# Optimization experiments

Hardware: AMD Instinct MI355X
Metric: run time of the kernel (lower is better)

## Reference

```python
import jax, jax.numpy as jnp
import numpy as np

N_NODES = 79
RAW_FEAT = 26
D_IN = RAW_FEAT + 6      # 32, in_channels after position concat
D_OUT = 2 * D_IN         # 64, out_channel_fac * in_channels
HIDDEN = 256
N_EDGES = 3000
BATCH = 256
POS_IDX = [120,124,128,132,136,140,144,148,152,237,241,245,249,253,257,261,265,269,354,358,362,366,370,374,378,382,386,471,475,479,483,487,491,495,499,503,588,592,596,600,604,608,612,616,620,705,709,713,717,721,725,729,733,737,822,826,830,834,838,842,846,850,854,48,53,60,67,73,157,352,388,583,586,817,901,906,913,920,926]


def _positions():
    width, height = 39, 25
    p = np.asarray(POS_IDX)
    xn = (p % width) / (width - 1)
    yn = (p // width) / (height - 1)
    feats = np.stack([xn, yn,
                      (np.sin(xn * 2 * np.pi) + 1) / 2,
                      (np.cos(xn * 2 * np.pi) + 1) / 2,
                      (np.sin(yn * 2 * np.pi) + 1) / 2,
                      (np.cos(yn * 2 * np.pi) + 1) / 2], axis=-1)
    return jnp.asarray(feats, jnp.float32)


def setup_inputs() -> dict:
    key = jax.random.key(0)
    ks = jax.random.split(key, 20)
    s = 0.05
    inp = {
        "state": jax.random.normal(ks[0], (BATCH, N_NODES, RAW_FEAT), jnp.float32),
        "pos_feat": _positions(),
        "edge_weights": jax.random.uniform(ks[1], (N_EDGES, 1), jnp.float32),
        # TransformerConv params (heads=1, edge_dim=1): torch Linear weights [out,in]
        "Wq": jax.random.normal(ks[2], (D_OUT, D_IN)) * s, "bq": jnp.zeros((D_OUT,)),
        "Wk": jax.random.normal(ks[3], (D_OUT, D_IN)) * s, "bk": jnp.zeros((D_OUT,)),
        "Wv": jax.random.normal(ks[4], (D_OUT, D_IN)) * s, "bv": jnp.zeros((D_OUT,)),
        "We": jax.random.normal(ks[5], (D_OUT, 1)) * s,            # lin_edge, bias=False
        "Wskip": jax.random.normal(ks[6], (D_OUT, D_IN)) * s, "bskip": jnp.zeros((D_OUT,)),
        # MLP head
        "W1": jax.random.normal(ks[7], (HIDDEN, D_IN + D_OUT + 1)) * s, "b1": jnp.zeros((HIDDEN,)),
        "g1": jnp.ones((HIDDEN,)), "beta1": jnp.zeros((HIDDEN,)),
        "W2": jax.random.normal(ks[8], (HIDDEN, HIDDEN)) * s, "b2": jnp.zeros((HIDDEN,)),
        "g2": jnp.ones((HIDDEN,)), "beta2": jnp.zeros((HIDDEN,)),
        "W3": jax.random.normal(ks[9], (1, HIDDEN)) * s, "b3": jnp.zeros((1,)),
        "edge_index": jax.random.randint(ks[10], (2, N_EDGES), 0, N_NODES, jnp.int32),
    }
    return inp


def _layernorm(x, g, b):
    m = x.mean(-1, keepdims=True)
    v = ((x - m) ** 2).mean(-1, keepdims=True)
    return (x - m) / jnp.sqrt(v + 1e-5) * g + b


def reference(state, pos_feat, edge_weights, Wq, bq, Wk, bk, Wv, bv, We, Wskip, bskip,
              W1, b1, g1, beta1, W2, b2, g2, beta2, W3, b3, edge_index):
    B = state.shape[0]
    # concat normalized positional features (shared across batch)
    x = jnp.concatenate([state, jnp.broadcast_to(pos_feat, (B, N_NODES, 6))], -1)  # [B,N,D_IN]
    src, dst = edge_index[0], edge_index[1]
    e = edge_weights @ We.T  # [E, D_OUT] edge embedding, shared across batch
    scale = 1.0 / jnp.sqrt(jnp.float32(D_OUT))

    def conv_one(xg):  # TransformerConv, heads=1, concat, root_weight
        q = xg @ Wq.T + bq
        k = xg @ Wk.T + bk
        v = xg @ Wv.T + bv
        ke = k[src] + e                      # [E, D_OUT]
        ve = v[src] + e
        alpha = (q[dst] * ke).sum(-1) * scale  # [E]
        amax = jax.ops.segment_max(alpha, dst, num_segments=N_NODES)
        amax = jnp.where(jnp.isfinite(amax), amax, 0.0)
        ex = jnp.exp(alpha - amax[dst])
        den = jax.ops.segment_sum(ex, dst, num_segments=N_NODES)
        w = ex / (den[dst] + 1e-16)
        agg = jax.ops.segment_sum(ve * w[:, None], dst, num_segments=N_NODES)
        return agg + xg @ Wskip.T + bskip

    out1 = jax.nn.relu(jax.vmap(conv_one)(x))  # [B,N,D_OUT]
    total_agents = x[..., 1].sum(-1)[:, None, None]  # [B,1,1]
    h = jnp.concatenate([out1, jnp.broadcast_to(total_agents, (B, N_NODES, 1)), x], -1)
    h = jax.nn.leaky_relu(_layernorm(h @ W1.T + b1, g1, beta1))
    h = jax.nn.leaky_relu(_layernorm(h @ W2.T + b2, g2, beta2))
    conc = jax.nn.softplus(h @ W3.T + b3).squeeze(-1)  # [B,N]
    action = conc / (conc.sum(-1, keepdims=True) + 1e-20)  # deterministic path
    return action
```

## Files before the change

kernel.cpp:

```cpp
#include <hip/hip_runtime.h>
#include <hip/hip_bf16.h>

#define N_NODES 79
#define RAW_FEAT 26
#define D_IN 32
#define D_OUT 64
#define HIDDEN 256
#define N_EDGES 3000
#define BATCH 256
#define M_ROWS (BATCH * N_NODES)
#define K1PAD 112

__global__ __launch_bounds__(256) void k_prep(
    const float* __restrict__ W1, const float* __restrict__ W2,
    const int* __restrict__ ei, const float* __restrict__ ew,
    const float* __restrict__ Wq, const float* __restrict__ Wk,
    const float* __restrict__ Wv, const float* __restrict__ Wsk,
    const float* __restrict__ bq, const float* __restrict__ bk,
    const float* __restrict__ bv, const float* __restrict__ bsk,
    float* __restrict__ W1t, float* __restrict__ W2t,
    float* __restrict__ Wall_t, float* __restrict__ ball,
    int* __restrict__ rp, int* __restrict__ csr_src,
    int* __restrict__ csr_dst, float* __restrict__ csr_ew)
{
    __shared__ float tile[64][65];
    __shared__ int cnt[N_NODES];
    __shared__ int base[N_NODES + 1];
    const int tid = threadIdx.x, bid = blockIdx.x;

    if (bid < 24) {
        const float* in; float* out; int C, Kpad, kb, rb;
        if (bid < 8) { in = W1; out = W1t; C = 97; Kpad = K1PAD;
                       kb = (bid & 1) * 64; rb = (bid >> 1) * 64; }
        else         { int b = bid - 8; in = W2; out = W2t; C = 256; Kpad = 256;
                       kb = (b & 3) * 64; rb = (b >> 2) * 64; }
        for (int i = tid; i < 4096; i += 256) {
            int rr = i >> 6, kk = i & 63;
            int r = rb + rr, k = kb + kk;
            tile[rr][kk] = (k < C) ? in[r * C + k] : 0.f;
        }
        __syncthreads();
        for (int i = tid; i < 4096; i += 256) {
            int kk = i >> 6, rr = i & 63;
            int k = kb + kk, r = rb + rr;
            if (k < Kpad) out[(size_t)k * HIDDEN + r] = tile[rr][kk];
        }
        return;
    }

    if (bid == 25) {
        for (int t = tid; t < 32 * 256; t += 256) {
            int k = t >> 8, j = t & 255;
            float v;
            if (j < 64)       v = Wq [j * 32 + k];
            else if (j < 128) v = Wk [(j - 64) * 32 + k];
            else if (j < 192) v = Wv [(j - 128) * 32 + k];
            else              v = Wsk[(j - 192) * 32 + k];
            Wall_t[t] = v;
        }
        if (tid < 64) {
            ball[tid]       = bq[tid];
            ball[64 + tid]  = bk[tid];
            ball[128 + tid] = bv[tid];
            ball[192 + tid] = bsk[tid];
        }
        return;
    }

    if (tid < N_NODES) cnt[tid] = 0;
    __syncthreads();
    for (int e = tid; e < N_EDGES; e += 256) atomicAdd(&cnt[ei[N_EDGES + e]], 1);
    __syncthreads();
    if (tid == 0) {
        int run = 0;
        for (int n = 0; n < N_NODES; ++n) { base[n] = run; run += cnt[n]; }
        base[N_NODES] = run;
    }
    __syncthreads();
    if (tid < N_NODES + 1) rp[tid] = base[tid];
    if (tid < N_NODES) cnt[tid] = base[tid];
    __syncthreads();
    for (int e = tid; e < N_EDGES; e += 256) {
        int d = ei[N_EDGES + e];
        int p = atomicAdd(&cnt[d], 1);
        csr_src[p] = ei[e];
        csr_dst[p] = d;
        csr_ew[p]  = ew[e];
    }
}

#define DOT4(S, Aa, Bb) S += Aa.x * Bb.x + Aa.y * Bb.y + Aa.z * Bb.z + Aa.w * Bb.w;

__global__ __launch_bounds__(256) void k_qkv(
    const float* __restrict__ state, const float* __restrict__ pos,
    const float* __restrict__ Wall_t, const float* __restrict__ ball,
    float* __restrict__ qkvs)
{
    __shared__ __align__(16) float Ax[32 * 32];
    __shared__ __align__(16) float Ws[32 * 256];

    const int tid = threadIdx.x;
    const int cg = tid & 31;
    const int rg = tid >> 5;
    const int m0 = blockIdx.x * 32;

    for (int t = tid; t < 32 * 32; t += 256) {
        int r = t >> 5, k = t & 31;
        int m = m0 + r, n = m - (m / N_NODES) * N_NODES;
        Ax[t] = (k < RAW_FEAT) ? state[m * RAW_FEAT + k] : pos[n * 6 + (k - RAW_FEAT)];
    }
    {
        const float4* Wg4 = (const float4*)Wall_t;
        float4* Ws4w = (float4*)Ws;
        #pragma unroll
        for (int i = 0; i < 8; ++i) Ws4w[tid + 256 * i] = Wg4[tid + 256 * i];
    }
    __syncthreads();

    float4 accL0 = {0,0,0,0}, accL1 = {0,0,0,0}, accL2 = {0,0,0,0}, accL3 = {0,0,0,0};
    float4 accH0 = {0,0,0,0}, accH1 = {0,0,0,0}, accH2 = {0,0,0,0}, accH3 = {0,0,0,0};
    const float4* Ax4 = (const float4*)Ax;
    const float4* Ws4 = (const float4*)Ws;

#define QSTEP(COMP, KS) { \
    float4 wL = Ws4[(kq * 4 + KS) * 64 + cg]; \
    float4 wH = Ws4[(kq * 4 + KS) * 64 + 32 + cg]; \
    accL0.x += a0.COMP * wL.x; accL0.y += a0.COMP * wL.y; accL0.z += a0.COMP * wL.z; accL0.w += a0.COMP * wL.w; \
    accL1.x += a1.COMP * wL.x; accL1.y += a1.COMP * wL.y; accL1.z += a1.COMP * wL.z; accL1.w += a1.COMP * wL.w; \
    accL2.x += a2.COMP * wL.x; accL2.y += a2.COMP * wL.y; accL2.z += a2.COMP * wL.z; accL2.w += a2.COMP * wL.w; \
    accL3.x += a3.COMP * wL.x; accL3.y += a3.COMP * wL.y; accL3.z += a3.COMP * wL.z; accL3.w += a3.COMP * wL.w; \
    accH0.x += a0.COMP * wH.x; accH0.y += a0.COMP * wH.y; accH0.z += a0.COMP * wH.z; accH0.w += a0.COMP * wH.w; \
    accH1.x += a1.COMP * wH.x; accH1.y += a1.COMP * wH.y; accH1.z += a1.COMP * wH.z; accH1.w += a1.COMP * wH.w; \
    accH2.x += a2.COMP * wH.x; accH2.y += a2.COMP * wH.y; accH2.z += a2.COMP * wH.z; accH2.w += a2.COMP * wH.w; \
    accH3.x += a3.COMP * wH.x; accH3.y += a3.COMP * wH.y; accH3.z += a3.COMP * wH.z; accH3.w += a3.COMP * wH.w; }

    #pragma unroll
    for (int kq = 0; kq < 8; ++kq) {
        float4 a0 = Ax4[(rg * 4 + 0) * 8 + kq];
        float4 a1 = Ax4[(rg * 4 + 1) * 8 + kq];
        float4 a2 = Ax4[(rg * 4 + 2) * 8 + kq];
        float4 a3 = Ax4[(rg * 4 + 3) * 8 + kq];
        QSTEP(x, 0)
        QSTEP(y, 1)
        QSTEP(z, 2)
        QSTEP(w, 3)
    }
#undef QSTEP

    {
        float4 bL = ((const float4*)ball)[cg];
        float4 bH = ((const float4*)ball)[32 + cg];
        float4* o4 = (float4*)qkvs;
#define QOUT(ACCL, ACCH, RR) { \
        float4 vL, vH; \
        vL.x = ACCL.x + bL.x; vL.y = ACCL.y + bL.y; vL.z = ACCL.z + bL.z; vL.w = ACCL.w + bL.w; \
        vH.x = ACCH.x + bH.x; vH.y = ACCH.y + bH.y; vH.z = ACCH.z + bH.z; vH.w = ACCH.w + bH.w; \
        o4[(size_t)(m0 + rg * 4 + RR) * 64 + cg] = vL; \
        o4[(size_t)(m0 + rg * 4 + RR) * 64 + 32 + cg] = vH; }
        QOUT(accL0, accH0, 0)
        QOUT(accL1, accH1, 1)
        QOUT(accL2, accH2, 2)
        QOUT(accL3, accH3, 3)
#undef QOUT
    }
}

__global__ __launch_bounds__(512) void k1_conv(
    const float* __restrict__ state, const float* __restrict__ qkvs,
    const int* __restrict__ rp_g, const int* __restrict__ csrc_g,
    const int* __restrict__ cdst_g, const float* __restrict__ cew_g,
    const float* __restrict__ We,
    float* __restrict__ out1_ws, float* __restrict__ ta_ws)
{
    __shared__ __align__(16) float qs [80 * 68];
    __shared__ __align__(16) float kss[80 * 68];
    __shared__ __align__(16) float vss[80 * 68];
    __shared__ __align__(16) float o1s[N_NODES * 68];
    __shared__ __align__(16) float SA[80 * 80];
    __shared__ __align__(16) float alpha[N_EDGES];
    __shared__ __align__(16) float ewc[N_EDGES];
    __shared__ unsigned short srcs[N_EDGES], dsts[N_EDGES];
    __shared__ __align__(16) float eW[64];
    __shared__ int   rp_s[80];
    __shared__ float qWe[80], csum_s[80];
    __shared__ float red80[80];

    const int b = blockIdx.x, tid = threadIdx.x;

    {
        const float4* qk4 = (const float4*)qkvs;
        for (int t = tid; t < N_NODES * 64; t += 512) {
            int n = t >> 6, j = t & 63;
            float4 v = qk4[(size_t)(b * N_NODES + n) * 64 + j];
            if (j < 16)      ((float4*)qs )[n * 17 + j]        = v;
            else if (j < 32) ((float4*)kss)[n * 17 + (j - 16)] = v;
            else if (j < 48) ((float4*)vss)[n * 17 + (j - 32)] = v;
            else             ((float4*)o1s)[n * 17 + (j - 48)] = v;
        }
    }
    for (int t = tid; t < N_EDGES; t += 512) {
        srcs[t] = (unsigned short)csrc_g[t];
        dsts[t] = (unsigned short)cdst_g[t];
        ewc[t]  = cew_g[t];
    }
    if (tid < 64) eW[tid] = We[tid];
    if (tid < 80) rp_s[tid] = rp_g[tid];
    if (tid < 79) red80[tid] = state[(b * N_NODES + tid) * RAW_FEAT + 1];
    if (tid == 79) red80[79] = 0.f;
    for (int t = tid; t < 68; t += 512) {
        qs[79 * 68 + t] = 0.f; kss[79 * 68 + t] = 0.f; vss[79 * 68 + t] = 0.f;
    }
    __syncthreads();

    for (int off = 64; off >= 1; off >>= 1) {
        if (tid < off && tid + off < 80) red80[tid] += red80[tid + off];
        __syncthreads();
    }
    if (tid == 0) ta_ws[b] = red80[0];

    if (tid < N_NODES) {
        const float4* q4 = (const float4*)(qs + tid * 68);
        const float4* e4 = (const float4*)eW;
        float s = 0.f;
        #pragma unroll
        for (int i = 0; i < 16; ++i) {
            float4 a = q4[i], e = e4[i];
            DOT4(s, a, e)
        }
        qWe[tid] = s;
    }
    __syncthreads();

    {
        const int rg = tid >> 5, cgp = tid & 31;
        const int r0 = rg * 5;
        int c0 = cgp * 3; if (c0 > 76) c0 = 76;
        float s00 = 0, s01 = 0, s02 = 0;
        float s10 = 0, s11 = 0, s12 = 0;
        float s20 = 0, s21 = 0, s22 = 0;
        float s30 = 0, s31 = 0, s32 = 0;
        float s40 = 0, s41 = 0, s42 = 0;
        const float4* q4p = (const float4*)qs;
        const float4* k4p = (const float4*)kss;
        for (int k4 = 0; k4 < 16; ++k4) {
            float4 q0 = q4p[(r0 + 0) * 17 + k4];
            float4 q1 = q4p[(r0 + 1) * 17 + k4];
            float4 q2 = q4p[(r0 + 2) * 17 + k4];
            float4 q3 = q4p[(r0 + 3) * 17 + k4];
            float4 q4v = q4p[(r0 + 4) * 17 + k4];
            float4 c0v = k4p[(c0 + 0) * 17 + k4];
            float4 c1v = k4p[(c0 + 1) * 17 + k4];
            float4 c2v = k4p[(c0 + 2) * 17 + k4];
            DOT4(s00, q0, c0v)  DOT4(s01, q0, c1v)  DOT4(s02, q0, c2v)
            DOT4(s10, q1, c0v)  DOT4(s11, q1, c1v)  DOT4(s12, q1, c2v)
            DOT4(s20, q2, c0v)  DOT4(s21, q2, c1v)  DOT4(s22, q2, c2v)
            DOT4(s30, q3, c0v)  DOT4(s31, q3, c1v)  DOT4(s32, q3, c2v)
            DOT4(s40, q4v, c0v) DOT4(s41, q4v, c1v) DOT4(s42, q4v, c2v)
        }
        SA[(r0 + 0) * 80 + c0 + 0] = s00; SA[(r0 + 0) * 80 + c0 + 1] = s01; SA[(r0 + 0) * 80 + c0 + 2] = s02;
        SA[(r0 + 1) * 80 + c0 + 0] = s10; SA[(r0 + 1) * 80 + c0 + 1] = s11; SA[(r0 + 1) * 80 + c0 + 2] = s12;
        SA[(r0 + 2) * 80 + c0 + 0] = s20; SA[(r0 + 2) * 80 + c0 + 1] = s21; SA[(r0 + 2) * 80 + c0 + 2] = s22;
        SA[(r0 + 3) * 80 + c0 + 0] = s30; SA[(r0 + 3) * 80 + c0 + 1] = s31; SA[(r0 + 3) * 80 + c0 + 2] = s32;
        SA[(r0 + 4) * 80 + c0 + 0] = s40; SA[(r0 + 4) * 80 + c0 + 1] = s41; SA[(r0 + 4) * 80 + c0 + 2] = s42;
    }
    __syncthreads();

    for (int t = tid; t < N_EDGES; t += 512) {
        int s = srcs[t], d = dsts[t];
        alpha[t] = 0.125f * (SA[d * 80 + s] + ewc[t] * qWe[d]);
    }
    __syncthreads();

    for (int t = tid; t < 6400; t += 512) SA[t] = 0.f;
    __syncthreads();

    if (tid < N_NODES) {
        int e0 = rp_s[tid], e1 = rp_s[tid + 1];
        float m = -1e30f;
        for (int e = e0; e < e1; ++e) m = fmaxf(m, alpha[e]);
        float s = 0.f, cs = 0.f;
        for (int e = e0; e < e1; ++e) {
            float ex = expf(alpha[e] - m);
            alpha[e] = ex;
            s += ex; cs += ex * ewc[e];
        }
        float rden = 1.f / (s + 1e-16f);
        csum_s[tid] = cs * rden;
        float* Ar = SA + tid * 80;
        for (int e = e0; e < e1; ++e) Ar[srcs[e]] += alpha[e] * rden;
    }
    __syncthreads();

    {
        const int rowg = tid >> 4, colg = tid & 15;
        int n0 = rowg * 3; if (n0 > 76) n0 = 76;
        float4 g0 = {0.f, 0.f, 0.f, 0.f};
        float4 g1 = {0.f, 0.f, 0.f, 0.f};
        float4 g2 = {0.f, 0.f, 0.f, 0.f};
        const float4* A4  = (const float4*)SA;
        const float4* v4p = (const float4*)vss;

#define AGGSTEP(COMP, SS) { \
        float4 vv = v4p[(s4 * 4 + SS) * 17 + colg]; \
        g0.x += a0.COMP * vv.x; g0.y += a0.COMP * vv.y; g0.z += a0.COMP * vv.z; g0.w += a0.COMP * vv.w; \
        g1.x += a1.COMP * vv.x; g1.y += a1.COMP * vv.y; g1.z += a1.COMP * vv.z; g1.w += a1.COMP * vv.w; \
        g2.x += a2.COMP * vv.x; g2.y += a2.COMP * vv.y; g2.z += a2.COMP * vv.z; g2.w += a2.COMP * vv.w; }

        for (int s4 = 0; s4 < 20; ++s4) {
            float4 a0 = A4[(n0 + 0) * 20 + s4];
            float4 a1 = A4[(n0 + 1) * 20 + s4];
            float4 a2 = A4[(n0 + 2) * 20 + s4];
            AGGSTEP(x, 0)
            AGGSTEP(y, 1)
            AGGSTEP(z, 2)
            AGGSTEP(w, 3)
        }
#undef AGGSTEP

        const float4* o4 = (const float4*)o1s;
        const float4* e4 = (const float4*)eW;
        float4 ev = e4[colg];

#define AGGOUT(GI, I) { int n = n0 + I; if (n < N_NODES) { \
        float4 sk = o4[n * 17 + colg]; float cs = csum_s[n]; float4 r; \
        r.x = fmaxf(sk.x + GI.x + cs * ev.x, 0.f); \
        r.y = fmaxf(sk.y + GI.y + cs * ev.y, 0.f); \
        r.z = fmaxf(sk.z + GI.z + cs * ev.z, 0.f); \
        r.w = fmaxf(sk.w + GI.w + cs * ev.w, 0.f); \
        ((float4*)out1_ws)[((size_t)b * N_NODES + n) * 16 + colg] = r; } }

        AGGOUT(g0, 0)
        AGGOUT(g1, 1)
        AGGOUT(g2, 2)
#undef AGGOUT
    }
}

__global__ __launch_bounds__(256) void k23_mlp(
    const float* __restrict__ state, const float* __restrict__ pos,
    const float* __restrict__ out1_ws, const float* __restrict__ ta_ws,
    const float* __restrict__ W1t, const float* __restrict__ b1,
    const float* __restrict__ g1, const float* __restrict__ be1,
    const float* __restrict__ W2t, const float* __restrict__ b2,
    const float* __restrict__ g2, const float* __restrict__ be2,
    const float* __restrict__ W3, const float* __restrict__ b3,
    float* __restrict__ conc_ws)
{
    __shared__ __align__(16) float A1[32 * K1PAD];
    __shared__ __align__(16) float A2[32 * 256];
    __shared__ __align__(16) float Ws[16 * 256];

    const int tid = threadIdx.x;
    const int cg = tid & 31;
    const int rg = tid >> 5;
    const int m0 = blockIdx.x * 32;

    const float4* W1t4 = (const float4*)W1t;
    const float4* W2t4 = (const float4*)W2t;
    const float4* A1_4 = (const float4*)A1;
    const float4* A2_4 = (const float4*)A2;
    float4* Ws4w = (float4*)Ws;
    const float4* Ws4 = (const float4*)Ws;

    for (int t = tid; t < 32 * K1PAD; t += 256) {
        int r = t / K1PAD, k = t - r * K1PAD;
        int m = m0 + r;
        float v = 0.f;
        if (k < 64)       v = out1_ws[m * 64 + k];
        else if (k == 64) v = ta_ws[m / N_NODES];
        else if (k < 91)  v = state[m * RAW_FEAT + (k - 65)];
        else if (k < 97)  { int n = m - (m / N_NODES) * N_NODES;
                            v = pos[n * 6 + (k - 91)]; }
        A1[t] = v;
    }
    float4 pre0 = W1t4[tid];
    float4 pre1 = W1t4[tid + 256];
    float4 pre2 = W1t4[tid + 512];
    float4 pre3 = W1t4[tid + 768];
    __syncthreads();

    float4 accL0 = {0,0,0,0}, accL1 = {0,0,0,0}, accL2 = {0,0,0,0}, accL3 = {0,0,0,0};
    float4 accH0 = {0,0,0,0}, accH1 = {0,0,0,0}, accH2 = {0,0,0,0}, accH3 = {0,0,0,0};

#define KSTEP(COMP, KS) { \
    float4 wL = Ws4[(kq * 4 + KS) * 64 + cg]; \
    float4 wH = Ws4[(kq * 4 + KS) * 64 + 32 + cg]; \
    accL0.x += a0.COMP * wL.x; accL0.y += a0.COMP * wL.y; accL0.z += a0.COMP * wL.z; accL0.w += a0.COMP * wL.w; \
    accL1.x += a1.COMP * wL.x; accL1.y += a1.COMP * wL.y; accL1.z += a1.COMP * wL.z; accL1.w += a1.COMP * wL.w; \
    accL2.x += a2.COMP * wL.x; accL2.y += a2.COMP * wL.y; accL2.z += a2.COMP * wL.z; accL2.w += a2.COMP * wL.w; \
    accL3.x += a3.COMP * wL.x; accL3.y += a3.COMP * wL.y; accL3.z += a3.COMP * wL.z; accL3.w += a3.COMP * wL.w; \
    accH0.x += a0.COMP * wH.x; accH0.y += a0.COMP * wH.y; accH0.z += a0.COMP * wH.z; accH0.w += a0.COMP * wH.w; \
    accH1.x += a1.COMP * wH.x; accH1.y += a1.COMP * wH.y; accH1.z += a1.COMP * wH.z; accH1.w += a1.COMP * wH.w; \
    accH2.x += a2.COMP * wH.x; accH2.y += a2.COMP * wH.y; accH2.z += a2.COMP * wH.z; accH2.w += a2.COMP * wH.w; \
    accH3.x += a3.COMP * wH.x; accH3.y += a3.COMP * wH.y; accH3.z += a3.COMP * wH.z; accH3.w += a3.COMP * wH.w; }

    for (int ch = 0; ch < 7; ++ch) {
        Ws4w[tid] = pre0; Ws4w[tid + 256] = pre1;
        Ws4w[tid + 512] = pre2; Ws4w[tid + 768] = pre3;
        __syncthreads();
        if (ch < 6) {
            pre0 = W1t4[(ch + 1) * 1024 + tid];
            pre1 = W1t4[(ch + 1) * 1024 + tid + 256];
            pre2 = W1t4[(ch + 1) * 1024 + tid + 512];
            pre3 = W1t4[(ch + 1) * 1024 + tid + 768];
        } else {
            pre0 = W2t4[tid];
            pre1 = W2t4[tid + 256];
            pre2 = W2t4[tid + 512];
            pre3 = W2t4[tid + 768];
        }
        #pragma unroll
        for (int kq = 0; kq < 4; ++kq) {
            float4 a0 = A1_4[(rg * 4 + 0) * 28 + ch * 4 + kq];
            float4 a1 = A1_4[(rg * 4 + 1) * 28 + ch * 4 + kq];
            float4 a2 = A1_4[(rg * 4 + 2) * 28 + ch * 4 + kq];
            float4 a3 = A1_4[(rg * 4 + 3) * 28 + ch * 4 + kq];
            KSTEP(x, 0)
            KSTEP(y, 1)
            KSTEP(z, 2)
            KSTEP(w, 3)
        }
        __syncthreads();
    }

    {
        float4 bL = ((const float4*)b1)[cg],  bH = ((const float4*)b1)[32 + cg];
        float4 gL = ((const float4*)g1)[cg],  gH = ((const float4*)g1)[32 + cg];
        float4 eL = ((const float4*)be1)[cg], eH = ((const float4*)be1)[32 + cg];

#define LN1_ROW(AL, AH, RR) { \
        float v0 = AL.x + bL.x, v1 = AL.y + bL.y, v2 = AL.z + bL.z, v3 = AL.w + bL.w; \
        float v4 = AH.x + bH.x, v5 = AH.y + bH.y, v6 = AH.z + bH.z, v7 = AH.w + bH.w; \
        float sm = v0 + v1 + v2 + v3 + v4 + v5 + v6 + v7; \
        float sq = v0*v0 + v1*v1 + v2*v2 + v3*v3 + v4*v4 + v5*v5 + v6*v6 + v7*v7; \
        for (int off = 16; off >= 1; off >>= 1) { sm += __shfl_xor(sm, off, 64); sq += __shfl_xor(sq, off, 64); } \
        float mu = sm * (1.f / 256.f), rstd = rsqrtf(sq * (1.f / 256.f) - mu * mu + 1e-5f); \
        float4 yL, yH; \
        yL.x = (v0 - mu) * rstd * gL.x + eL.x; yL.y = (v1 - mu) * rstd * gL.y + eL.y; \
        yL.z = (v2 - mu) * rstd * gL.z + eL.z; yL.w = (v3 - mu) * rstd * gL.w + eL.w; \
        yH.x = (v4 - mu) * rstd * gH.x + eH.x; yH.y = (v5 - mu) * rstd * gH.y + eH.y; \
        yH.z = (v6 - mu) * rstd * gH.z + eH.z; yH.w = (v7 - mu) * rstd * gH.w + eH.w; \
        yL.x = yL.x > 0.f ? yL.x : 0.01f * yL.x; yL.y = yL.y > 0.f ? yL.y : 0.01f * yL.y; \
        yL.z = yL.z > 0.f ? yL.z : 0.01f * yL.z; yL.w = yL.w > 0.f ? yL.w : 0.01f * yL.w; \
        yH.x = yH.x > 0.f ? yH.x : 0.01f * yH.x; yH.y = yH.y > 0.f ? yH.y : 0.01f * yH.y; \
        yH.z = yH.z > 0.f ? yH.z : 0.01f * yH.z; yH.w = yH.w > 0.f ? yH.w : 0.01f * yH.w; \
        ((float4*)A2)[(rg * 4 + RR) * 64 + cg] = yL; \
        ((float4*)A2)[(rg * 4 + RR) * 64 + 32 + cg] = yH; }

        LN1_ROW(accL0, accH0, 0)
        LN1_ROW(accL1, accH1, 1)
        LN1_ROW(accL2, accH2, 2)
        LN1_ROW(accL3, accH3, 3)
#undef LN1_ROW
        accL0 = {0,0,0,0}; accL1 = {0,0,0,0}; accL2 = {0,0,0,0}; accL3 = {0,0,0,0};
        accH0 = {0,0,0,0}; accH1 = {0,0,0,0}; accH2 = {0,0,0,0}; accH3 = {0,0,0,0};
    }

    for (int ch = 0; ch < 16; ++ch) {
        Ws4w[tid] = pre0; Ws4w[tid + 256] = pre1;
        Ws4w[tid + 512] = pre2; Ws4w[tid + 768] = pre3;
        __syncthreads();
        if (ch < 15) {
            pre0 = W2t4[(ch + 1) * 1024 + tid];
            pre1 = W2t4[(ch + 1) * 1024 + tid + 256];
            pre2 = W2t4[(ch + 1) * 1024 + tid + 512];
            pre3 = W2t4[(ch + 1) * 1024 + tid + 768];
        }
        #pragma unroll
        for (int kq = 0; kq < 4; ++kq) {
            float4 a0 = A2_4[(rg * 4 + 0) * 64 + ch * 4 + kq];
            float4 a1 = A2_4[(rg * 4 + 1) * 64 + ch * 4 + kq];
            float4 a2 = A2_4[(rg * 4 + 2) * 64 + ch * 4 + kq];
            float4 a3 = A2_4[(rg * 4 + 3) * 64 + ch * 4 + kq];
            KSTEP(x, 0)
            KSTEP(y, 1)
            KSTEP(z, 2)
            KSTEP(w, 3)
        }
        __syncthreads();
    }
#undef KSTEP

    {
        float4 bL = ((const float4*)b2)[cg],  bH = ((const float4*)b2)[32 + cg];
        float4 gL = ((const float4*)g2)[cg],  gH = ((const float4*)g2)[32 + cg];
        float4 eL = ((const float4*)be2)[cg], eH = ((const float4*)be2)[32 + cg];
        float4 wL3 = ((const float4*)W3)[cg], wH3 = ((const float4*)W3)[32 + cg];
        float bb3 = b3[0];

#define LN2_ROW(AL, AH, RR) { \
        float v0 = AL.x + bL.x, v1 = AL.y + bL.y, v2 = AL.z + bL.z, v3 = AL.w + bL.w; \
        float v4 = AH.x + bH.x, v5 = AH.y + bH.y, v6 = AH.z + bH.z, v7 = AH.w + bH.w; \
        float sm = v0 + v1 + v2 + v3 + v4 + v5 + v6 + v7; \
        float sq = v0*v0 + v1*v1 + v2*v2 + v3*v3 + v4*v4 + v5*v5 + v6*v6 + v7*v7; \
        for (int off = 16; off >= 1; off >>= 1) { sm += __shfl_xor(sm, off, 64); sq += __shfl_xor(sq, off, 64); } \
        float mu = sm * (1.f / 256.f), rstd = rsqrtf(sq * (1.f / 256.f) - mu * mu + 1e-5f); \
        float z0 = (v0 - mu) * rstd * gL.x + eL.x, z1 = (v1 - mu) * rstd * gL.y + eL.y; \
        float z2 = (v2 - mu) * rstd * gL.z + eL.z, z3 = (v3 - mu) * rstd * gL.w + eL.w; \
        float z4 = (v4 - mu) * rstd * gH.x + eH.x, z5 = (v5 - mu) * rstd * gH.y + eH.y; \
        float z6 = (v6 - mu) * rstd * gH.z + eH.z, z7 = (v7 - mu) * rstd * gH.w + eH.w; \
        z0 = z0 > 0.f ? z0 : 0.01f * z0; z1 = z1 > 0.f ? z1 : 0.01f * z1; \
        z2 = z2 > 0.f ? z2 : 0.01f * z2; z3 = z3 > 0.f ? z3 : 0.01f * z3; \
        z4 = z4 > 0.f ? z4 : 0.01f * z4; z5 = z5 > 0.f ? z5 : 0.01f * z5; \
        z6 = z6 > 0.f ? z6 : 0.01f * z6; z7 = z7 > 0.f ? z7 : 0.01f * z7; \
        float part = z0 * wL3.x + z1 * wL3.y + z2 * wL3.z + z3 * wL3.w \
                   + z4 * wH3.x + z5 * wH3.y + z6 * wH3.z + z7 * wH3.w; \
        for (int off = 16; off >= 1; off >>= 1) part += __shfl_xor(part, off, 64); \
        if (cg == 0) { float x = part + bb3; \
            conc_ws[m0 + rg * 4 + RR] = fmaxf(x, 0.f) + log1pf(expf(-fabsf(x))); } }

        LN2_ROW(accL0, accH0, 0)
        LN2_ROW(accL1, accH1, 1)
        LN2_ROW(accL2, accH2, 2)
        LN2_ROW(accL3, accH3, 3)
#undef LN2_ROW
    }
}

__global__ __launch_bounds__(128) void k4_norm(
    const float* __restrict__ conc_ws, float* __restrict__ out)
{
    __shared__ float red[128];
    const int b = blockIdx.x, tid = threadIdx.x;
    float v = 0.f;
    if (tid < N_NODES) v = conc_ws[b * N_NODES + tid];
    red[tid] = v;
    __syncthreads();
    for (int off = 64; off >= 1; off >>= 1) {
        if (tid < off) red[tid] += red[tid + off];
        __syncthreads();
    }
    float s = red[0];
    if (tid < N_NODES) out[b * N_NODES + tid] = v / (s + 1e-20f);
}

extern "C" void kernel_launch(void* const* d_in, const int* in_sizes, int n_in,
                              void* d_out, int out_size, void* d_ws, size_t ws_size,
                              hipStream_t stream) {
    const float* state = (const float*)d_in[0];
    const float* pos   = (const float*)d_in[1];
    const float* ew    = (const float*)d_in[2];
    const float* Wq  = (const float*)d_in[3];  const float* bq  = (const float*)d_in[4];
    const float* Wk  = (const float*)d_in[5];  const float* bk  = (const float*)d_in[6];
    const float* Wv  = (const float*)d_in[7];  const float* bv  = (const float*)d_in[8];
    const float* We  = (const float*)d_in[9];
    const float* Wsk = (const float*)d_in[10]; const float* bsk = (const float*)d_in[11];
    const float* W1  = (const float*)d_in[12]; const float* b1  = (const float*)d_in[13];
    const float* g1  = (const float*)d_in[14]; const float* be1 = (const float*)d_in[15];
    const float* W2  = (const float*)d_in[16]; const float* b2  = (const float*)d_in[17];
    const float* g2  = (const float*)d_in[18]; const float* be2 = (const float*)d_in[19];
    const float* W3  = (const float*)d_in[20]; const float* b3  = (const float*)d_in[21];
    const int*   ei  = (const int*)d_in[22];

    float* ws    = (float*)d_ws;
    float* ta    = ws;
    float* out1  = ws + 256;
    float* conc  = out1 + (size_t)M_ROWS * 64;
    float* W1t   = conc + M_ROWS;
    float* W2t   = W1t + K1PAD * HIDDEN;
    float* Wall  = W2t + HIDDEN * HIDDEN;
    float* ball  = Wall + 32 * 256;
    float* qkvs  = ball + 256;
    int*   rp    = (int*)(qkvs + (size_t)M_ROWS * 256);
    int*   csrc  = rp + 80;
    int*   cdst  = csrc + N_EDGES;
    float* cew   = (float*)(cdst + N_EDGES);
    float* out   = (float*)d_out;

    k_prep<<<dim3(26), dim3(256), 0, stream>>>(
        W1, W2, ei, ew, Wq, Wk, Wv, Wsk, bq, bk, bv, bsk,
        W1t, W2t, Wall, ball, rp, csrc, cdst, cew);
    k_qkv<<<dim3(M_ROWS / 32), dim3(256), 0, stream>>>(
        state, pos, Wall, ball, qkvs);
    k1_conv<<<dim3(BATCH), dim3(512), 0, stream>>>(
        state, qkvs, rp, csrc, cdst, cew, We, out1, ta);
    k23_mlp<<<dim3(M_ROWS / 32), dim3(256), 0, stream>>>(
        state, pos, out1, ta, W1t, b1, g1, be1,
        W2t, b2, g2, be2, W3, b3, conc);
    k4_norm<<<dim3(BATCH), dim3(128), 0, stream>>>(conc, out);
}
```

Measured before the change: 235.5 us.

## Fuse QKV projection into graph conv kernel and alias shared buffers

Removes the separate k_qkv kernel and computes the Q/K/V/skip projections inside k1_conv per batch block. Each block loads the block's node features and the weights into a shared union buffer that is later reused for SA and alpha. This drops one kernel launch and the write and re-read of a roughly 20 MB qkvs intermediate. It also merges A1/A2 in k23_mlp into one buffer to cut shared memory use. In exchange the projection runs on only 256 blocks with a simple per-thread GEMV loop, so it gets less parallelism than the standalone kernel had.

```diff
diff --git a/kernel.cpp b/kernel.cpp
--- a/kernel.cpp
+++ b/kernel.cpp
@@ -91,82 +91,9 @@
 
 #define DOT4(S, Aa, Bb) S += Aa.x * Bb.x + Aa.y * Bb.y + Aa.z * Bb.z + Aa.w * Bb.w;
 
-__global__ __launch_bounds__(256) void k_qkv(
+__global__ __launch_bounds__(512) void k1_conv(
     const float* __restrict__ state, const float* __restrict__ pos,
     const float* __restrict__ Wall_t, const float* __restrict__ ball,
-    float* __restrict__ qkvs)
-{
-    __shared__ __align__(16) float Ax[32 * 32];
-    __shared__ __align__(16) float Ws[32 * 256];
-
-    const int tid = threadIdx.x;
-    const int cg = tid & 31;
-    const int rg = tid >> 5;
-    const int m0 = blockIdx.x * 32;
-
-    for (int t = tid; t < 32 * 32; t += 256) {
-        int r = t >> 5, k = t & 31;
-        int m = m0 + r, n = m - (m / N_NODES) * N_NODES;
-        Ax[t] = (k < RAW_FEAT) ? state[m * RAW_FEAT + k] : pos[n * 6 + (k - RAW_FEAT)];
-    }
-    {
-        const float4* Wg4 = (const float4*)Wall_t;
-        float4* Ws4w = (float4*)Ws;
-        #pragma unroll
-        for (int i = 0; i < 8; ++i) Ws4w[tid + 256 * i] = Wg4[tid + 256 * i];
-    }
-    __syncthreads();
-
-    float4 accL0 = {0,0,0,0}, accL1 = {0,0,0,0}, accL2 = {0,0,0,0}, accL3 = {0,0,0,0};
-    float4 accH0 = {0,0,0,0}, accH1 = {0,0,0,0}, accH2 = {0,0,0,0}, accH3 = {0,0,0,0};
-    const float4* Ax4 = (const float4*)Ax;
-    const float4* Ws4 = (const float4*)Ws;
-
-#define QSTEP(COMP, KS) { \
-    float4 wL = Ws4[(kq * 4 + KS) * 64 + cg]; \
-    float4 wH = Ws4[(kq * 4 + KS) * 64 + 32 + cg]; \
-    accL0.x += a0.COMP * wL.x; accL0.y += a0.COMP * wL.y; accL0.z += a0.COMP * wL.z; accL0.w += a0.COMP * wL.w; \
-    accL1.x += a1.COMP * wL.x; accL1.y += a1.COMP * wL.y; accL1.z += a1.COMP * wL.z; accL1.w += a1.COMP * wL.w; \
-    accL2.x += a2.COMP * wL.x; accL2.y += a2.COMP * wL.y; accL2.z += a2.COMP * wL.z; accL2.w += a2.COMP * wL.w; \
-    accL3.x += a3.COMP * wL.x; accL3.y += a3.COMP * wL.y; accL3.z += a3.COMP * wL.z; accL3.w += a3.COMP * wL.w; \
-    accH0.x += a0.COMP * wH.x; accH0.y += a0.COMP * wH.y; accH0.z += a0.COMP * wH.z; accH0.w += a0.COMP * wH.w; \
-    accH1.x += a1.COMP * wH.x; accH1.y += a1.COMP * wH.y; accH1.z += a1.COMP * wH.z; accH1.w += a1.COMP * wH.w; \
-    accH2.x += a2.COMP * wH.x; accH2.y += a2.COMP * wH.y; accH2.z += a2.COMP * wH.z; accH2.w += a2.COMP * wH.w; \
-    accH3.x += a3.COMP * wH.x; accH3.y += a3.COMP * wH.y; accH3.z += a3.COMP * wH.z; accH3.w += a3.COMP * wH.w; }
-
-    #pragma unroll
-    for (int kq = 0; kq < 8; ++kq) {
-        float4 a0 = Ax4[(rg * 4 + 0) * 8 + kq];
-        float4 a1 = Ax4[(rg * 4 + 1) * 8 + kq];
-        float4 a2 = Ax4[(rg * 4 + 2) * 8 + kq];
-        float4 a3 = Ax4[(rg * 4 + 3) * 8 + kq];
-        QSTEP(x, 0)
-        QSTEP(y, 1)
-        QSTEP(z, 2)
-        QSTEP(w, 3)
-    }
-#undef QSTEP
-
-    {
-        float4 bL = ((const float4*)ball)[cg];
-        float4 bH = ((const float4*)ball)[32 + cg];
-        float4* o4 = (float4*)qkvs;
-#define QOUT(ACCL, ACCH, RR) { \
-        float4 vL, vH; \
-        vL.x = ACCL.x + bL.x; vL.y = ACCL.y + bL.y; vL.z = ACCL.z + bL.z; vL.w = ACCL.w + bL.w; \
-        vH.x = ACCH.x + bH.x; vH.y = ACCH.y + bH.y; vH.z = ACCH.z + bH.z; vH.w = ACCH.w + bH.w; \
-        o4[(size_t)(m0 + rg * 4 + RR) * 64 + cg] = vL; \
-        o4[(size_t)(m0 + rg * 4 + RR) * 64 + 32 + cg] = vH; }
-        QOUT(accL0, accH0, 0)
-        QOUT(accL1, accH1, 1)
-        QOUT(accL2, accH2, 2)
-        QOUT(accL3, accH3, 3)
-#undef QOUT
-    }
-}
-
-__global__ __launch_bounds__(512) void k1_conv(
-    const float* __restrict__ state, const float* __restrict__ qkvs,
     const int* __restrict__ rp_g, const int* __restrict__ csrc_g,
     const int* __restrict__ cdst_g, const float* __restrict__ cew_g,
     const float* __restrict__ We,
@@ -176,8 +103,7 @@
     __shared__ __align__(16) float kss[80 * 68];
     __shared__ __align__(16) float vss[80 * 68];
     __shared__ __align__(16) float o1s[N_NODES * 68];
-    __shared__ __align__(16) float SA[80 * 80];
-    __shared__ __align__(16) float alpha[N_EDGES];
+    __shared__ __align__(16) char uni[43904];
     __shared__ __align__(16) float ewc[N_EDGES];
     __shared__ unsigned short srcs[N_EDGES], dsts[N_EDGES];
     __shared__ __align__(16) float eW[64];
@@ -185,19 +111,25 @@
     __shared__ float qWe[80], csum_s[80];
     __shared__ float red80[80];
 
+    float* xs     = (float*)uni;
+    float* Wall_s = (float*)(uni + 10112);
+    float* ball_s = (float*)(uni + 42880);
+    float* SA     = (float*)uni;
+    float* alpha  = (float*)(uni + 25600);
+
     const int b = blockIdx.x, tid = threadIdx.x;
 
+    for (int t = tid; t < N_NODES * 32; t += 512) {
+        int n = t >> 5, c = t & 31;
+        xs[t] = (c < RAW_FEAT) ? state[(b * N_NODES + n) * RAW_FEAT + c]
+                               : pos[n * 6 + (c - RAW_FEAT)];
+    }
     {
-        const float4* qk4 = (const float4*)qkvs;
-        for (int t = tid; t < N_NODES * 64; t += 512) {
-            int n = t >> 6, j = t & 63;
-            float4 v = qk4[(size_t)(b * N_NODES + n) * 64 + j];
-            if (j < 16)      ((float4*)qs )[n * 17 + j]        = v;
-            else if (j < 32) ((float4*)kss)[n * 17 + (j - 16)] = v;
-            else if (j < 48) ((float4*)vss)[n * 17 + (j - 32)] = v;
-            else             ((float4*)o1s)[n * 17 + (j - 48)] = v;
-        }
-    }
+        const float4* Wg4 = (const float4*)Wall_t;
+        float4* Ws4w = (float4*)Wall_s;
+        for (int t = tid; t < 2048; t += 512) Ws4w[t] = Wg4[t];
+    }
+    if (tid < 256) ball_s[tid] = ball[tid];
     for (int t = tid; t < N_EDGES; t += 512) {
         srcs[t] = (unsigned short)csrc_g[t];
         dsts[t] = (unsigned short)cdst_g[t];
@@ -212,12 +144,38 @@
     }
     __syncthreads();
 
+    {
+        const float4* xs4 = (const float4*)xs;
+        const float4* W4  = (const float4*)Wall_s;
+        const float4* b4  = (const float4*)ball_s;
+        for (int t = tid; t < N_NODES * 64; t += 512) {
+            int n = t >> 6, c4 = t & 63;
+            float4 acc = b4[c4];
+            #pragma unroll
+            for (int k4 = 0; k4 < 8; ++k4) {
+                float4 xv = xs4[n * 8 + k4];
+                float4 w0 = W4[(k4 * 4 + 0) * 64 + c4];
+                float4 w1 = W4[(k4 * 4 + 1) * 64 + c4];
+                float4 w2 = W4[(k4 * 4 + 2) * 64 + c4];
+                float4 w3 = W4[(k4 * 4 + 3) * 64 + c4];
+                acc.x += xv.x * w0.x + xv.y * w1.x + xv.z * w2.x + xv.w * w3.x;
+                acc.y += xv.x * w0.y + xv.y * w1.y + xv.z * w2.y + xv.w * w3.y;
+                acc.z += xv.x * w0.z + xv.y * w1.z + xv.z * w2.z + xv.w * w3.z;
+                acc.w += xv.x * w0.w + xv.y * w1.w + xv.z * w2.w + xv.w * w3.w;
+            }
+            if (c4 < 16)      ((float4*)qs )[n * 17 + c4]        = acc;
+            else if (c4 < 32) ((float4*)kss)[n * 17 + (c4 - 16)] = acc;
+            else if (c4 < 48) ((float4*)vss)[n * 17 + (c4 - 32)] = acc;
+            else              ((float4*)o1s)[n * 17 + (c4 - 48)] = acc;
+        }
+    }
+    __syncthreads();
+
     for (int off = 64; off >= 1; off >>= 1) {
         if (tid < off && tid + off < 80) red80[tid] += red80[tid + off];
         __syncthreads();
     }
     if (tid == 0) ta_ws[b] = red80[0];
-
     if (tid < N_NODES) {
         const float4* q4 = (const float4*)(qs + tid * 68);
         const float4* e4 = (const float4*)eW;
@@ -346,8 +304,7 @@
     const float* __restrict__ W3, const float* __restrict__ b3,
     float* __restrict__ conc_ws)
 {
-    __shared__ __align__(16) float A1[32 * K1PAD];
-    __shared__ __align__(16) float A2[32 * 256];
+    __shared__ __align__(16) float A12[32 * 256];
     __shared__ __align__(16) float Ws[16 * 256];
 
     const int tid = threadIdx.x;
@@ -357,8 +314,7 @@
 
     const float4* W1t4 = (const float4*)W1t;
     const float4* W2t4 = (const float4*)W2t;
-    const float4* A1_4 = (const float4*)A1;
-    const float4* A2_4 = (const float4*)A2;
+    const float4* A12_4 = (const float4*)A12;
     float4* Ws4w = (float4*)Ws;
     const float4* Ws4 = (const float4*)Ws;
 
@@ -371,7 +327,7 @@
         else if (k < 91)  v = state[m * RAW_FEAT + (k - 65)];
         else if (k < 97)  { int n = m - (m / N_NODES) * N_NODES;
                             v = pos[n * 6 + (k - 91)]; }
-        A1[t] = v;
+        A12[t] = v;
     }
     float4 pre0 = W1t4[tid];
     float4 pre1 = W1t4[tid + 256];
@@ -411,10 +367,10 @@
         }
         #pragma unroll
         for (int kq = 0; kq < 4; ++kq) {
-            float4 a0 = A1_4[(rg * 4 + 0) * 28 + ch * 4 + kq];
-            float4 a1 = A1_4[(rg * 4 + 1) * 28 + ch * 4 + kq];
-            float4 a2 = A1_4[(rg * 4 + 2) * 28 + ch * 4 + kq];
-            float4 a3 = A1_4[(rg * 4 + 3) * 28 + ch * 4 + kq];
+            float4 a0 = A12_4[(rg * 4 + 0) * 28 + ch * 4 + kq];
+            float4 a1 = A12_4[(rg * 4 + 1) * 28 + ch * 4 + kq];
+            float4 a2 = A12_4[(rg * 4 + 2) * 28 + ch * 4 + kq];
+            float4 a3 = A12_4[(rg * 4 + 3) * 28 + ch * 4 + kq];
             KSTEP(x, 0)
             KSTEP(y, 1)
             KSTEP(z, 2)
@@ -444,8 +400,8 @@
         yL.z = yL.z > 0.f ? yL.z : 0.01f * yL.z; yL.w = yL.w > 0.f ? yL.w : 0.01f * yL.w; \
         yH.x = yH.x > 0.f ? yH.x : 0.01f * yH.x; yH.y = yH.y > 0.f ? yH.y : 0.01f * yH.y; \
         yH.z = yH.z > 0.f ? yH.z : 0.01f * yH.z; yH.w = yH.w > 0.f ? yH.w : 0.01f * yH.w; \
-        ((float4*)A2)[(rg * 4 + RR) * 64 + cg] = yL; \
-        ((float4*)A2)[(rg * 4 + RR) * 64 + 32 + cg] = yH; }
+        ((float4*)A12)[(rg * 4 + RR) * 64 + cg] = yL; \
+        ((float4*)A12)[(rg * 4 + RR) * 64 + 32 + cg] = yH; }
 
         LN1_ROW(accL0, accH0, 0)
         LN1_ROW(accL1, accH1, 1)
@@ -468,10 +424,10 @@
         }
         #pragma unroll
         for (int kq = 0; kq < 4; ++kq) {
-            float4 a0 = A2_4[(rg * 4 + 0) * 64 + ch * 4 + kq];
-            float4 a1 = A2_4[(rg * 4 + 1) * 64 + ch * 4 + kq];
-            float4 a2 = A2_4[(rg * 4 + 2) * 64 + ch * 4 + kq];
-            float4 a3 = A2_4[(rg * 4 + 3) * 64 + ch * 4 + kq];
+            float4 a0 = A12_4[(rg * 4 + 0) * 64 + ch * 4 + kq];
+            float4 a1 = A12_4[(rg * 4 + 1) * 64 + ch * 4 + kq];
+            float4 a2 = A12_4[(rg * 4 + 2) * 64 + ch * 4 + kq];
+            float4 a3 = A12_4[(rg * 4 + 3) * 64 + ch * 4 + kq];
             KSTEP(x, 0)
             KSTEP(y, 1)
             KSTEP(z, 2)
@@ -560,8 +516,7 @@
     float* W2t   = W1t + K1PAD * HIDDEN;
     float* Wall  = W2t + HIDDEN * HIDDEN;
     float* ball  = Wall + 32 * 256;
-    float* qkvs  = ball + 256;
-    int*   rp    = (int*)(qkvs + (size_t)M_ROWS * 256);
+    int*   rp    = (int*)(ball + 256);
     int*   csrc  = rp + 80;
     int*   cdst  = csrc + N_EDGES;
     float* cew   = (float*)(cdst + N_EDGES);
@@ -570,10 +525,8 @@
     k_prep<<<dim3(26), dim3(256), 0, stream>>>(
         W1, W2, ei, ew, Wq, Wk, Wv, Wsk, bq, bk, bv, bsk,
         W1t, W2t, Wall, ball, rp, csrc, cdst, cew);
-    k_qkv<<<dim3(M_ROWS / 32), dim3(256), 0, stream>>>(
-        state, pos, Wall, ball, qkvs);
     k1_conv<<<dim3(BATCH), dim3(512), 0, stream>>>(
-        state, qkvs, rp, csrc, cdst, cew, We, out1, ta);
+        state, pos, Wall, ball, rp, csrc, cdst, cew, We, out1, ta);
     k23_mlp<<<dim3(M_ROWS / 32), dim3(256), 0, stream>>>(
         state, pos, out1, ta, W1t, b1, g1, be1,
         W2t, b2, g2, be2, W3, b3, conc);
```

Result: faster. 220.4 us (-6.4%).
